# Kernel optimization log

Measured on AMD Instinct MI355X. Metric: run time of the kernel, lower is better.

Reference implementation:

```python
import jax, jax.numpy as jnp
import numpy as np

L = 6  # num_objects (greedy iterations)
BIG = 1e8  # penalty for already-used template ids (matches torch code)


def setup_inputs() -> dict:
    key = jax.random.key(0)
    k1, k2, k3, k4 = jax.random.split(key, 4)
    B, T, C, H, W = 16, 144, 1, 128, 128
    x = jax.random.uniform(k1, (B, C, H, W), jnp.float32)
    templates = jax.random.uniform(k2, (B, T, C, H, W), jnp.float32)
    masks = jax.random.uniform(k3, (B, T, 1, H, W), jnp.float32)
    background = jax.random.uniform(k4, (1, C, H, W), jnp.float32)
    return {"x": x, "templates": templates, "masks": masks, "background": background}


def _greedy_select(x, templates, masks, background):
    """Greedy template selection. Faithful to DecompModel._greedy_selection
    (use_empty is falsy by default -> empty template = 5*ones, empty mask = ones).
    Key identity used for efficiency: dead-leaves composition of the l
    already-selected objects is affine in whatever lies below them:
        recons = A + Mprod * below,
    where A accumulates painted objects and Mprod = prod(1 - mask_i).
    The new candidate at step l is painted BELOW the existing selection
    (it sits at the last index, and compose_templates paints last->first),
    so below = cand*cand_mask + bg*(1-cand_mask). Identical math, no
    O(B*T*l) recomposition per step."""
    B, T = templates.shape[0], templates.shape[1]
    H, W = templates.shape[-2], templates.shape[-1]
    empty_t = 5.0 * jnp.ones((B, 1) + templates.shape[2:], templates.dtype)
    empty_m = jnp.ones((B, 1) + masks.shape[2:], masks.dtype)
    temps = jnp.concatenate([empty_t, templates], axis=1)   # (B,T+1,C,H,W)
    ms = jnp.concatenate([empty_m, masks], axis=1)           # (B,T+1,1,H,W)
    bg = jnp.broadcast_to(background, (B,) + background.shape[1:])  # (B,C,H,W)

    A0 = jnp.zeros_like(bg)                                  # painted-so-far
    M0 = jnp.ones((B, 1, H, W), bg.dtype)                    # transmission
    used0 = jnp.zeros((B, T + 1), bool)
    bidx = jnp.arange(B)

    def step(carry, _):
        A, Mprod, used = carry
        below = temps * ms + bg[:, None] * (1.0 - ms)        # (B,T+1,C,H,W)
        recons = A[:, None] + Mprod[:, None] * below         # (B,T+1,C,H,W)
        errors = jnp.mean((x[:, None] - recons) ** 2, axis=(2, 3, 4))  # (B,T+1)
        errors = jnp.where(used, BIG, errors)
        ids = jnp.argmin(errors, axis=1)                     # (B,)
        hit = (jnp.arange(T + 1)[None, :] == ids[:, None]) & (ids[:, None] != 0)
        used = used | hit                                    # empty id=0 reusable
        sel_t = temps[bidx, ids]                             # (B,C,H,W)
        sel_m = ms[bidx, ids]                                # (B,1,H,W)
        A = A + Mprod * sel_t * sel_m
        Mprod = Mprod * (1.0 - sel_m)
        return (A, Mprod, used), ids

    (_, _, _), ids = jax.lax.scan(step, (A0, M0, used0), None, length=L)
    ids = ids.T                                              # (B,L)
    objects = temps[bidx[:, None], ids]                      # (B,L,C,H,W)
    omasks = ms[bidx[:, None], ids]                          # (B,L,1,H,W)
    return objects, omasks, ids


def _compose(objects, omasks, background):
    """Dead-leaves composition, painting from last object to first
    (first selected object ends up on top), as in compose_templates."""
    B, N = objects.shape[0], objects.shape[1]
    recons = jnp.broadcast_to(background, (B,) + background.shape[1:])
    for i in range(N):  # small fixed loop over L objects
        o = objects[:, N - 1 - i]
        m = omasks[:, N - 1 - i]
        recons = o * m + recons * (1.0 - m)
    return recons


def reference(x, templates, masks, background):
    objects, omasks, ids = _greedy_select(x, templates, masks, background)
    recons = _compose(objects, omasks, background)           # (B,C,H,W)
    return recons, objects, omasks, ids
```

## Files before the change

kernel.cpp:

```cpp
#include <hip/hip_runtime.h>
#include <math.h>

#define BB 16
#define TT 144
#define TP1 145
#define HW4 4096
#define HW8 2048
#define LL 6
#define BIGE 1e30
#define EPSQ 7.62951e-6
#define RB 37
#define NBLK (BB * RB)
#define BCHUNK 74
#define RCHUNK 290

typedef float          f4    __attribute__((ext_vector_type(4)));
typedef float          f8    __attribute__((ext_vector_type(8)));
typedef unsigned short u16x4 __attribute__((ext_vector_type(4)));
typedef unsigned short u16x8 __attribute__((ext_vector_type(8)));

static const size_t OFF_MS   = 0;
static const size_t OFF_R    = 1u << 20;
static const size_t OFF_E32  = 2u << 20;
static const size_t OFF_E16  = (2u << 20) + 32768;
static const size_t OFF_D    = (2u << 20) + 65536;
static const size_t OFF_USED = (2u << 20) + 81920;
static const size_t OFF_WQ   = 3u << 20;
static const size_t WS_FULL  = OFF_WQ + 75497472ull;

__device__ __forceinline__ float hsum(f4 v) { return ((v.x + v.y) + v.z) + v.w; }
__device__ __forceinline__ float hsum8(f8 v) {
    return (((v.s0 + v.s1) + (v.s2 + v.s3)) + ((v.s4 + v.s5) + (v.s6 + v.s7)));
}
__device__ __forceinline__ f8 fabs8(f8 v) {
    f8 o;
    o.s0 = __builtin_fabsf(v.s0); o.s1 = __builtin_fabsf(v.s1);
    o.s2 = __builtin_fabsf(v.s2); o.s3 = __builtin_fabsf(v.s3);
    o.s4 = __builtin_fabsf(v.s4); o.s5 = __builtin_fabsf(v.s5);
    o.s6 = __builtin_fabsf(v.s6); o.s7 = __builtin_fabsf(v.s7);
    return o;
}

__device__ __forceinline__ double blk_reduce(double s) {
    for (int off = 32; off; off >>= 1) s += __shfl_down(s, off);
    __shared__ double smr[4];
    if ((threadIdx.x & 63) == 0) smr[threadIdx.x >> 6] = s;
    __syncthreads();
    return smr[0] + smr[1] + smr[2] + smr[3];
}

__device__ __forceinline__ void blk_reduce2(double& a, double& b) {
    for (int off = 32; off; off >>= 1) { a += __shfl_down(a, off); b += __shfl_down(b, off); }
    __shared__ double sa[4], sb[4];
    if ((threadIdx.x & 63) == 0) { sa[threadIdx.x >> 6] = a; sb[threadIdx.x >> 6] = b; }
    __syncthreads();
    a = sa[0] + sa[1] + sa[2] + sa[3];
    b = sb[0] + sb[1] + sb[2] + sb[3];
}

__device__ __forceinline__ void blk_reduce4(double s[4]) {
    for (int off = 32; off; off >>= 1) {
        s[0] += __shfl_down(s[0], off); s[1] += __shfl_down(s[1], off);
        s[2] += __shfl_down(s[2], off); s[3] += __shfl_down(s[3], off);
    }
    __shared__ double sm4[4][4];
    const int wv = threadIdx.x >> 6;
    if ((threadIdx.x & 63) == 0) {
        sm4[wv][0] = s[0]; sm4[wv][1] = s[1]; sm4[wv][2] = s[2]; sm4[wv][3] = s[3];
    }
    __syncthreads();
    for (int k = 0; k < 4; ++k) s[k] = sm4[0][k] + sm4[1][k] + sm4[2][k] + sm4[3][k];
}

__global__ void k_build(const f4* __restrict__ temps, const f4* __restrict__ masks,
                        const f4* __restrict__ bg, const f4* __restrict__ x,
                        u16x4* __restrict__ wq, double* __restrict__ err32,
                        int* __restrict__ used) {
    const int lin = blockIdx.x;
    const int wg = (lin & 7) * BCHUNK + (lin >> 3);
    const int b = wg / RB, rg = wg - b * RB;
    const int tid = threadIdx.x;
    const f4* xb = x + (size_t)b * HW4;
    if (rg == RB - 1) {
        if (tid < TP1) used[b * TP1 + tid] = 0;
        double s = 0.0;
        for (int j = tid; j < HW4; j += 256) {
            f4 d = 5.f - xb[j];
            s += (double)hsum(d * d);
        }
        double tot = blk_reduce(s);
        if (tid == 0) err32[b * TP1 + 0] = tot;
        return;
    }
    const int tbase = 1 + rg * 4;
    const size_t r0 = ((size_t)(b * TT + tbase - 1)) * HW4;
    const size_t r1 = r0 + HW4, r2 = r1 + HW4, r3 = r2 + HW4;
    double s[4] = {0.0, 0.0, 0.0, 0.0};
    #pragma unroll 2
    for (int j = tid; j < HW4; j += 256) {
        f4 bv = bg[j], xv = xb[j];
        f4 tv0 = __builtin_nontemporal_load(&temps[r0 + j]);
        f4 mv0 = __builtin_nontemporal_load(&masks[r0 + j]);
        f4 w0 = tv0 * mv0 + bv * (1.f - mv0);
        wq[r0 + j] = __builtin_convertvector(w0 * 65535.f + 0.5f, u16x4);
        f4 d0 = w0 - xv; s[0] += (double)hsum(d0 * d0);
        f4 tv1 = __builtin_nontemporal_load(&temps[r1 + j]);
        f4 mv1 = __builtin_nontemporal_load(&masks[r1 + j]);
        f4 w1 = tv1 * mv1 + bv * (1.f - mv1);
        wq[r1 + j] = __builtin_convertvector(w1 * 65535.f + 0.5f, u16x4);
        f4 d1 = w1 - xv; s[1] += (double)hsum(d1 * d1);
        f4 tv2 = __builtin_nontemporal_load(&temps[r2 + j]);
        f4 mv2 = __builtin_nontemporal_load(&masks[r2 + j]);
        f4 w2 = tv2 * mv2 + bv * (1.f - mv2);
        wq[r2 + j] = __builtin_convertvector(w2 * 65535.f + 0.5f, u16x4);
        f4 d2 = w2 - xv; s[2] += (double)hsum(d2 * d2);
        f4 tv3 = __builtin_nontemporal_load(&temps[r3 + j]);
        f4 mv3 = __builtin_nontemporal_load(&masks[r3 + j]);
        f4 w3 = tv3 * mv3 + bv * (1.f - mv3);
        wq[r3 + j] = __builtin_convertvector(w3 * 65535.f + 0.5f, u16x4);
        f4 d3 = w3 - xv; s[3] += (double)hsum(d3 * d3);
    }
    blk_reduce4(s);
    if (tid == 0)
        for (int k = 0; k < 4; ++k) err32[b * TP1 + tbase + k] = s[k];
}

__global__ void k_errs(const u16x8* __restrict__ wq,
                       const f8* __restrict__ Ms, const f8* __restrict__ R,
                       const int* __restrict__ used,
                       double* __restrict__ err16, double* __restrict__ Dd) {
    const int lin = blockIdx.x;
    const int wg = (lin & 7) * BCHUNK + (lin >> 3);
    const int b = wg / RB, rg = wg - b * RB;
    const int tid = threadIdx.x;
    const f8* msb = Ms + (size_t)b * HW8;
    const f8* rb  = R  + (size_t)b * HW8;
    if (rg == RB - 1) {
        double s = 0.0, d = 0.0;
        for (int j = tid; j < HW8; j += 256) {
            f8 ms = msb[j], rr = rb[j];
            f8 M = ms * 65535.f;
            f8 dd = M * 5.f - rr;
            s += (double)hsum8(dd * dd);
            d += (double)hsum8(M * (M + fabs8(rr)));
        }
        blk_reduce2(s, d);
        if (tid == 0) { err16[b * TP1 + 0] = s; Dd[b] = d; }
        return;
    }
    const int tbase = 1 + rg * 4;
    const size_t r0 = ((size_t)(b * TT + tbase - 1)) * HW8;
    const size_t r1 = r0 + HW8, r2 = r1 + HW8, r3 = r2 + HW8;
    double s[4] = {0.0, 0.0, 0.0, 0.0};
    #pragma unroll 2
    for (int j = tid; j < HW8; j += 256) {
        f8 ms = msb[j], rr = rb[j];
        f8 q0 = __builtin_convertvector(wq[r0 + j], f8);
        f8 d0 = q0 * ms - rr; s[0] += (double)hsum8(d0 * d0);
        f8 q1 = __builtin_convertvector(wq[r1 + j], f8);
        f8 d1 = q1 * ms - rr; s[1] += (double)hsum8(d1 * d1);
        f8 q2 = __builtin_convertvector(wq[r2 + j], f8);
        f8 d2 = q2 * ms - rr; s[2] += (double)hsum8(d2 * d2);
        f8 q3 = __builtin_convertvector(wq[r3 + j], f8);
        f8 d3 = q3 * ms - rr; s[3] += (double)hsum8(d3 * d3);
    }
    blk_reduce4(s);
    if (tid == 0)
        for (int k = 0; k < 4; ++k) {
            int t = tbase + k;
            err16[b * TP1 + t] = used[b * TP1 + t] ? BIGE : s[k];
        }
}

__global__ void k_refine(const f4* __restrict__ temps, const f4* __restrict__ masks,
                         const f4* __restrict__ bg,
                         const f4* __restrict__ Ms4, const f4* __restrict__ R4,
                         const double* __restrict__ err16, const double* __restrict__ Dd,
                         double* __restrict__ err32) {
    const int lin = blockIdx.x;
    const int wg = (lin & 7) * RCHUNK + (lin >> 3);
    const int b = wg / TP1, t = wg - b * TP1;
    const int tid = threadIdx.x;
    double e = (tid < TP1) ? err16[b * TP1 + tid] : 1e300;
    double m = e;
    for (int off = 32; off; off >>= 1) {
        double o = __shfl_down(m, off);
        m = (o < m) ? o : m;
    }
    __shared__ double sm[4]; __shared__ double smin_s; __shared__ int scnt[4];
    if ((tid & 63) == 0) sm[tid >> 6] = m;
    __syncthreads();
    if (tid == 0) {
        double a = (sm[0] < sm[1]) ? sm[0] : sm[1];
        double c = (sm[2] < sm[3]) ? sm[2] : sm[3];
        smin_s = (a < c) ? a : c;
    }
    __syncthreads();
    const double thr = smin_s + (6.0 * EPSQ * Dd[b] + 0.15);
    int flag = (tid < TP1) && (e <= thr);
    unsigned long long bal = __ballot(flag);
    if ((tid & 63) == 0) scnt[tid >> 6] = __popcll(bal);
    __syncthreads();
    const int cnt = scnt[0] + scnt[1] + scnt[2] + scnt[3];
    const double mys = err16[b * TP1 + t];
    if (mys > thr) { if (tid == 0) err32[b * TP1 + t] = BIGE; return; }
    if (cnt == 1 || t == 0) { if (tid == 0) err32[b * TP1 + t] = mys; return; }
    const size_t row = ((size_t)(b * TT + t - 1)) * HW4;
    const f4* msb = Ms4 + (size_t)b * HW4;
    const f4* rb  = R4  + (size_t)b * HW4;
    double s = 0.0;
    for (int j = tid; j < HW4; j += 256) {
        f4 tv = temps[row + j], mv = masks[row + j], bv = bg[j];
        f4 w = tv * mv + bv * (1.f - mv);
        f4 M = msb[j] * 65535.f;
        f4 d = w * M - rb[j];
        s += (double)hsum(d * d);
    }
    double tot = blk_reduce(s);
    if (tid == 0) err32[b * TP1 + t] = tot;
}

template <bool FIRST, bool LAST>
__global__ void k_upd(const f4* __restrict__ temps, const f4* __restrict__ masks,
                      const f4* __restrict__ x, const f4* __restrict__ bg,
                      const double* __restrict__ err,
                      int* __restrict__ used, f4* __restrict__ Ms4, f4* __restrict__ R4,
                      f4* __restrict__ out_obj, f4* __restrict__ out_msk,
                      f4* __restrict__ out_rec, float* __restrict__ out_ids, int l) {
    const int lin = blockIdx.x;
    const int wg = (lin & 7) * 32 + (lin >> 3);
    const int tid = threadIdx.x;
    const int gid = wg * 256 + tid;
    const int b = gid >> 12;
    const int p = gid & (HW4 - 1);
    __shared__ int ssel;
    if (tid < 64) {
        double best = 1e301; int bi = TP1;
        for (int t = tid; t < TP1; t += 64) {
            double e = err[b * TP1 + t];
            if (e < best) { best = e; bi = t; }
        }
        for (int off = 32; off; off >>= 1) {
            double oe = __shfl_down(best, off);
            int    oi = __shfl_down(bi, off);
            if (oe < best || (oe == best && oi < bi)) { best = oe; bi = oi; }
        }
        if (tid == 0) ssel = bi;
    }
    __syncthreads();
    const int id = ssel;
    f4 st, sm_;
    if (id == 0) { st = (f4){5.f,5.f,5.f,5.f}; sm_ = (f4){1.f,1.f,1.f,1.f}; }
    else {
        size_t base = ((size_t)(b * TT + id - 1)) * HW4 + p;
        st = temps[base]; sm_ = masks[base];
    }
    f4 xv = x[gid];
    f4 a, mp;
    if (FIRST) { a = (f4){0.f,0.f,0.f,0.f}; mp = (f4){1.f,1.f,1.f,1.f}; }
    else       { mp = Ms4[gid] * 65535.f; a = xv - R4[gid]; }
    a = a + mp * st * sm_;
    mp = mp * (1.f - sm_);
    const size_t ob = ((size_t)(b * LL + l)) * HW4 + p;
    out_obj[ob] = st;
    out_msk[ob] = sm_;
    if (LAST) {
        out_rec[gid] = a + mp * bg[p];
    } else {
        Ms4[gid] = mp * (1.f / 65535.f);
        R4[gid]  = xv - a;
    }
    if ((wg & 15) == 0 && tid == 0) {
        if (id != 0) used[b * TP1 + id] = 1;
        out_ids[b * LL + l] = (float)id;
    }
}

__global__ void k_init0(const f4* __restrict__ x, f4* __restrict__ Ms4, f4* __restrict__ R4,
                        int* __restrict__ used) {
    int gid = blockIdx.x * blockDim.x + threadIdx.x;
    if (gid < BB * TP1) used[gid] = 0;
    if (gid >= BB * HW4) return;
    float msv = (float)(1.0 / 65535.0);
    Ms4[gid] = (f4){msv, msv, msv, msv};
    R4[gid] = x[gid];
}

__global__ void k_errfb(const f4* __restrict__ temps, const f4* __restrict__ masks,
                        const f4* __restrict__ bg,
                        const f4* __restrict__ Ms4, const f4* __restrict__ R4,
                        const int* __restrict__ used, double* __restrict__ err32) {
    const int lin = blockIdx.x;
    const int wg = (lin & 7) * RCHUNK + (lin >> 3);
    const int b = wg / TP1, t = wg - b * TP1;
    const int tid = threadIdx.x;
    if (t != 0 && used[b * TP1 + t]) {
        if (tid == 0) err32[b * TP1 + t] = BIGE;
        return;
    }
    const f4* msb = Ms4 + (size_t)b * HW4;
    const f4* rb  = R4  + (size_t)b * HW4;
    double s = 0.0;
    if (t == 0) {
        for (int j = tid; j < HW4; j += 256) {
            f4 M = msb[j] * 65535.f;
            f4 d = M * 5.f - rb[j];
            s += (double)hsum(d * d);
        }
    } else {
        const size_t row = ((size_t)(b * TT + t - 1)) * HW4;
        for (int j = tid; j < HW4; j += 256) {
            f4 tv = temps[row + j], mv = masks[row + j], bv = bg[j];
            f4 w = tv * mv + bv * (1.f - mv);
            f4 M = msb[j] * 65535.f;
            f4 d = w * M - rb[j];
            s += (double)hsum(d * d);
        }
    }
    double tot = blk_reduce(s);
    if (tid == 0) err32[b * TP1 + t] = tot;
}

extern "C" void kernel_launch(void* const* d_in, const int* in_sizes, int n_in,
                              void* d_out, int out_size, void* d_ws, size_t ws_size,
                              hipStream_t stream) {
    const f4* x     = (const f4*)d_in[0];
    const f4* temps = (const f4*)d_in[1];
    const f4* masks = (const f4*)d_in[2];
    const f4* bg    = (const f4*)d_in[3];

    float* out      = (float*)d_out;
    f4*    out_rec  = (f4*)out;
    f4*    out_obj  = (f4*)(out + 262144);
    f4*    out_msk  = (f4*)(out + 262144 + 1572864);
    float* out_ids  = out + 262144 + 2 * 1572864;

    char* ws = (char*)d_ws;
    f4*     Ms4   = (f4*)(ws + OFF_MS);
    f4*     R4    = (f4*)(ws + OFF_R);
    double* err32 = (double*)(ws + OFF_E32);
    double* err16 = (double*)(ws + OFF_E16);
    double* Dd    = (double*)(ws + OFF_D);
    int*    used  = (int*)(ws + OFF_USED);
    u16x4*  wq    = (u16x4*)(ws + OFF_WQ);

    const bool full = (ws_size >= WS_FULL);

    if (full) {
        k_build<<<NBLK, 256, 0, stream>>>(temps, masks, bg, x, wq, err32, used);
        k_upd<true, false><<<256, 256, 0, stream>>>(temps, masks, x, bg, err32, used,
                                                    Ms4, R4, out_obj, out_msk, out_rec, out_ids, 0);
        for (int l = 1; l < LL; ++l) {
            k_errs<<<NBLK, 256, 0, stream>>>((const u16x8*)wq, (const f8*)Ms4, (const f8*)R4,
                                             used, err16, Dd);
            k_refine<<<BB * TP1, 256, 0, stream>>>(temps, masks, bg, Ms4, R4, err16, Dd, err32);
            if (l < LL - 1)
                k_upd<false, false><<<256, 256, 0, stream>>>(temps, masks, x, bg, err32, used,
                                                             Ms4, R4, out_obj, out_msk, out_rec, out_ids, l);
            else
                k_upd<false, true><<<256, 256, 0, stream>>>(temps, masks, x, bg, err32, used,
                                                            Ms4, R4, out_obj, out_msk, out_rec, out_ids, l);
        }
    } else {
        k_init0<<<(BB * HW4 + 255) / 256, 256, 0, stream>>>(x, Ms4, R4, used);
        for (int l = 0; l < LL; ++l) {
            k_errfb<<<BB * TP1, 256, 0, stream>>>(temps, masks, bg, Ms4, R4, used, err32);
            if (l == 0)
                k_upd<true, false><<<256, 256, 0, stream>>>(temps, masks, x, bg, err32, used,
                                                            Ms4, R4, out_obj, out_msk, out_rec, out_ids, l);
            else if (l == LL - 1)
                k_upd<false, true><<<256, 256, 0, stream>>>(temps, masks, x, bg, err32, used,
                                                            Ms4, R4, out_obj, out_msk, out_rec, out_ids, l);
            else
                k_upd<false, false><<<256, 256, 0, stream>>>(temps, masks, x, bg, err32, used,
                                                             Ms4, R4, out_obj, out_msk, out_rec, out_ids, l);
        }
    }
}
```

Before: 240.4 us.

## Fuse state update with quantized error pass and resolve argmin per batch

Each greedy step used to run three launches: quantized error, refine and update. These become two: a per-batch resolve kernel picks the argmin, refines near-ties exactly and zeroes the accumulators, and a fused kernel applies the selected object to the state and, in the same pass, accumulates the next step's quantized errors for all templates through atomic adds. This removes a launch per step and the reread of the state buffers. It relies on double-precision atomics and on one block per batch for the tie refinement, which could serialize if many candidates fall within the threshold.

```diff
diff --git a/kernel.cpp b/kernel.cpp
--- a/kernel.cpp
+++ b/kernel.cpp
@@ -6,6 +6,7 @@
 #define TP1 145
 #define HW4 4096
 #define HW8 2048
+#define HWF2 8192
 #define LL 6
 #define BIGE 1e30
 #define EPSQ 7.62951e-6
@@ -18,13 +19,15 @@
 typedef float          f8    __attribute__((ext_vector_type(8)));
 typedef unsigned short u16x4 __attribute__((ext_vector_type(4)));
 typedef unsigned short u16x8 __attribute__((ext_vector_type(8)));
-
-static const size_t OFF_MS   = 0;
+typedef unsigned long long ull;
+
+static const size_t OFF_M    = 0;
 static const size_t OFF_R    = 1u << 20;
 static const size_t OFF_E32  = 2u << 20;
 static const size_t OFF_E16  = (2u << 20) + 32768;
 static const size_t OFF_D    = (2u << 20) + 65536;
 static const size_t OFF_USED = (2u << 20) + 81920;
+static const size_t OFF_SEL  = (2u << 20) + 98304;
 static const size_t OFF_WQ   = 3u << 20;
 static const size_t WS_FULL  = OFF_WQ + 75497472ull;
 
@@ -41,12 +44,19 @@
     return o;
 }
 
+__device__ __forceinline__ double wave_reduce_d(double s) {
+    for (int off = 32; off; off >>= 1) s += __shfl_down(s, off);
+    return s;
+}
+
 __device__ __forceinline__ double blk_reduce(double s) {
     for (int off = 32; off; off >>= 1) s += __shfl_down(s, off);
     __shared__ double smr[4];
     if ((threadIdx.x & 63) == 0) smr[threadIdx.x >> 6] = s;
     __syncthreads();
-    return smr[0] + smr[1] + smr[2] + smr[3];
+    double r = smr[0] + smr[1] + smr[2] + smr[3];
+    __syncthreads();
+    return r;
 }
 
 __device__ __forceinline__ void blk_reduce2(double& a, double& b) {
@@ -56,6 +66,7 @@
     __syncthreads();
     a = sa[0] + sa[1] + sa[2] + sa[3];
     b = sb[0] + sb[1] + sb[2] + sb[3];
+    __syncthreads();
 }
 
 __device__ __forceinline__ void blk_reduce4(double s[4]) {
@@ -125,112 +136,228 @@
         for (int k = 0; k < 4; ++k) err32[b * TP1 + tbase + k] = s[k];
 }
 
-__global__ void k_errs(const u16x8* __restrict__ wq,
-                       const f8* __restrict__ Ms, const f8* __restrict__ R,
-                       const int* __restrict__ used,
-                       double* __restrict__ err16, double* __restrict__ Dd) {
+template <bool EXACT>
+__global__ void k_resolve(const f4* __restrict__ temps, const f4* __restrict__ masks,
+                          const f4* __restrict__ bg,
+                          const f4* __restrict__ Mst, const f4* __restrict__ Rst,
+                          const double* __restrict__ scr, double* __restrict__ zbuf,
+                          double* __restrict__ Dd, int* __restrict__ used,
+                          int* __restrict__ selp, float* __restrict__ out_ids, int l) {
+    const int b = blockIdx.x;
+    const int tid = threadIdx.x;
+    const double* sb = scr + (size_t)b * TP1;
+    __shared__ int s_sel, s_cnt;
+    __shared__ ull s_mask[3];
+    if (tid < 64) {
+        double e0 = sb[tid];
+        double e1 = (tid + 64 < TP1) ? sb[tid + 64] : 1e301;
+        double e2 = (tid + 128 < TP1) ? sb[tid + 128] : 1e301;
+        if (!EXACT) {
+            if (tid != 0 && used[b * TP1 + tid]) e0 = BIGE;
+            if (tid + 64 < TP1 && used[b * TP1 + tid + 64]) e1 = BIGE;
+            if (tid + 128 < TP1 && used[b * TP1 + tid + 128]) e2 = BIGE;
+        }
+        double best = e0; int bi = tid;
+        if (e1 < best) { best = e1; bi = tid + 64; }
+        if (e2 < best) { best = e2; bi = tid + 128; }
+        for (int off = 32; off; off >>= 1) {
+            double oe = __shfl_down(best, off);
+            int    oi = __shfl_down(bi, off);
+            if (oe < best || (oe == best && oi < bi)) { best = oe; bi = oi; }
+        }
+        best = __shfl(best, 0); bi = __shfl(bi, 0);
+        if (EXACT) {
+            if (tid == 0) { s_sel = bi; s_cnt = 1; }
+        } else {
+            const double thr = best + (6.0 * EPSQ * Dd[b] + 0.15);
+            ull m0 = __ballot(e0 <= thr);
+            ull m1 = __ballot(e1 <= thr);
+            ull m2 = __ballot(e2 <= thr);
+            if (tid == 0) {
+                s_mask[0] = m0; s_mask[1] = m1; s_mask[2] = m2;
+                s_cnt = __popcll(m0) + __popcll(m1) + __popcll(m2);
+                s_sel = bi;
+            }
+        }
+    }
+    __syncthreads();
+    if (!EXACT && s_cnt > 1) {
+        __shared__ double s_beste; __shared__ int s_besti;
+        if (tid == 0) { s_beste = 1e301; s_besti = -1; }
+        __syncthreads();
+        const f4* Mb = Mst + (size_t)b * HW4;
+        const f4* Rb = Rst + (size_t)b * HW4;
+        for (int t = 0; t < TP1; ++t) {
+            if (!((s_mask[t >> 6] >> (t & 63)) & 1ull)) continue;
+            double s;
+            if (t == 0) {
+                s = sb[0];
+            } else {
+                const size_t row = ((size_t)(b * TT + t - 1)) * HW4;
+                double acc = 0.0;
+                for (int j = tid; j < HW4; j += 256) {
+                    f4 tv = temps[row + j], mv = masks[row + j], bv = bg[j];
+                    f4 w = tv * mv + bv * (1.f - mv);
+                    f4 d = w * Mb[j] - Rb[j];
+                    acc += (double)hsum(d * d);
+                }
+                s = blk_reduce(acc);
+            }
+            if (tid == 0 && s < s_beste) { s_beste = s; s_besti = t; }
+            __syncthreads();
+        }
+        if (tid == 0) s_sel = s_besti;
+        __syncthreads();
+    }
+    const int sel = s_sel;
+    if (tid == 0) {
+        selp[b] = sel;
+        out_ids[b * LL + l] = (float)sel;
+        if (sel != 0) used[b * TP1 + sel] = 1;
+        Dd[b] = 0.0;
+    }
+    for (int t = tid; t < TP1; t += 256) zbuf[(size_t)b * TP1 + t] = 0.0;
+}
+
+template <bool FIRST, bool LAST>
+__global__ __launch_bounds__(256) void k_fused(
+    const float2* __restrict__ temps2, const float2* __restrict__ masks2,
+    const float2* __restrict__ x2, const float2* __restrict__ bg2,
+    const u16x8* __restrict__ wq, const int* __restrict__ selp,
+    float2* __restrict__ Mst2, float2* __restrict__ Rst2,
+    double* __restrict__ err16, double* __restrict__ Dd,
+    float2* __restrict__ out_obj2, float2* __restrict__ out_msk2,
+    float2* __restrict__ out_rec2, int l) {
     const int lin = blockIdx.x;
-    const int wg = (lin & 7) * BCHUNK + (lin >> 3);
-    const int b = wg / RB, rg = wg - b * RB;
+    const int wg = (lin & 7) * 64 + (lin >> 3);
+    const int b = wg >> 5;
+    const int s = wg & 31;
     const int tid = threadIdx.x;
-    const f8* msb = Ms + (size_t)b * HW8;
-    const f8* rb  = R  + (size_t)b * HW8;
-    if (rg == RB - 1) {
-        double s = 0.0, d = 0.0;
-        for (int j = tid; j < HW8; j += 256) {
-            f8 ms = msb[j], rr = rb[j];
-            f8 M = ms * 65535.f;
-            f8 dd = M * 5.f - rr;
-            s += (double)hsum8(dd * dd);
-            d += (double)hsum8(M * (M + fabs8(rr)));
-        }
-        blk_reduce2(s, d);
-        if (tid == 0) { err16[b * TP1 + 0] = s; Dd[b] = d; }
+    const int sel = selp[b];
+    const int P = s * 512;
+    const size_t g2 = (size_t)b * HWF2 + (P >> 1) + tid;
+
+    float2 xv = x2[g2];
+    float2 st, sm;
+    if (sel == 0) { st = make_float2(5.f, 5.f); sm = make_float2(1.f, 1.f); }
+    else {
+        size_t base2 = ((size_t)(b * TT + sel - 1)) * HWF2 + (P >> 1) + tid;
+        st = temps2[base2]; sm = masks2[base2];
+    }
+    float2 a, mp;
+    if (FIRST) { a = make_float2(0.f, 0.f); mp = make_float2(1.f, 1.f); }
+    else {
+        mp = Mst2[g2];
+        float2 rr0 = Rst2[g2];
+        a = make_float2(xv.x - rr0.x, xv.y - rr0.y);
+    }
+    a.x += mp.x * st.x * sm.x;  mp.x *= (1.f - sm.x);
+    a.y += mp.y * st.y * sm.y;  mp.y *= (1.f - sm.y);
+    const size_t ob2 = ((size_t)(b * LL + l)) * HWF2 + (P >> 1) + tid;
+    out_obj2[ob2] = st;
+    out_msk2[ob2] = sm;
+    if (LAST) {
+        float2 bv = bg2[(P >> 1) + tid];
+        out_rec2[g2] = make_float2(a.x + mp.x * bv.x, a.y + mp.y * bv.y);
         return;
     }
-    const int tbase = 1 + rg * 4;
-    const size_t r0 = ((size_t)(b * TT + tbase - 1)) * HW8;
-    const size_t r1 = r0 + HW8, r2 = r1 + HW8, r3 = r2 + HW8;
-    double s[4] = {0.0, 0.0, 0.0, 0.0};
-    #pragma unroll 2
-    for (int j = tid; j < HW8; j += 256) {
-        f8 ms = msb[j], rr = rb[j];
-        f8 q0 = __builtin_convertvector(wq[r0 + j], f8);
-        f8 d0 = q0 * ms - rr; s[0] += (double)hsum8(d0 * d0);
-        f8 q1 = __builtin_convertvector(wq[r1 + j], f8);
-        f8 d1 = q1 * ms - rr; s[1] += (double)hsum8(d1 * d1);
-        f8 q2 = __builtin_convertvector(wq[r2 + j], f8);
-        f8 d2 = q2 * ms - rr; s[2] += (double)hsum8(d2 * d2);
-        f8 q3 = __builtin_convertvector(wq[r3 + j], f8);
-        f8 d3 = q3 * ms - rr; s[3] += (double)hsum8(d3 * d3);
-    }
-    blk_reduce4(s);
-    if (tid == 0)
-        for (int k = 0; k < 4; ++k) {
-            int t = tbase + k;
-            err16[b * TP1 + t] = used[b * TP1 + t] ? BIGE : s[k];
-        }
-}
-
-__global__ void k_refine(const f4* __restrict__ temps, const f4* __restrict__ masks,
-                         const f4* __restrict__ bg,
-                         const f4* __restrict__ Ms4, const f4* __restrict__ R4,
-                         const double* __restrict__ err16, const double* __restrict__ Dd,
-                         double* __restrict__ err32) {
+    float2 rr = make_float2(xv.x - a.x, xv.y - a.y);
+    Mst2[g2] = mp;
+    Rst2[g2] = rr;
+    float d0x = 5.f * mp.x - rr.x, d0y = 5.f * mp.y - rr.y;
+    double t0 = (double)(d0x * d0x + d0y * d0y);
+    double dD = (double)(mp.x * (mp.x + __builtin_fabsf(rr.x)) +
+                         mp.y * (mp.y + __builtin_fabsf(rr.y)));
+    blk_reduce2(t0, dD);
+    if (tid == 0) {
+        atomicAdd(&err16[(size_t)b * TP1 + 0], t0);
+        atomicAdd(&Dd[b], dD);
+    }
+    __shared__ float lms[512], lr[512];
+    lms[tid * 2]     = mp.x * (1.f / 65535.f);
+    lms[tid * 2 + 1] = mp.y * (1.f / 65535.f);
+    lr[tid * 2]      = rr.x;
+    lr[tid * 2 + 1]  = rr.y;
+    __syncthreads();
+    const int lane = tid & 63, w = tid >> 6;
+    float ms8[8], r8[8];
+    #pragma unroll
+    for (int k = 0; k < 8; ++k) { ms8[k] = lms[lane * 8 + k]; r8[k] = lr[lane * 8 + k]; }
+    const size_t rowbase = (size_t)b * TT * HW8 + (size_t)(P >> 3) + lane;
+    double* eb = err16 + (size_t)b * TP1 + 1;
+    for (int t = w; t < TT; t += 8) {
+        u16x8 qa = wq[rowbase + (size_t)t * HW8];
+        u16x8 qb = wq[rowbase + (size_t)(t + 4) * HW8];
+        f8 fa = __builtin_convertvector(qa, f8);
+        f8 fb = __builtin_convertvector(qb, f8);
+        float ga = 0.f, gb = 0.f;
+        #pragma unroll
+        for (int k = 0; k < 8; ++k) {
+            float da = fa[k] * ms8[k] - r8[k];
+            float db = fb[k] * ms8[k] - r8[k];
+            ga += da * da;
+            gb += db * db;
+        }
+        double sa = wave_reduce_d((double)ga);
+        double sb = wave_reduce_d((double)gb);
+        if (lane == 0) {
+            atomicAdd(&eb[t], sa);
+            atomicAdd(&eb[t + 4], sb);
+        }
+    }
+}
+
+__global__ void k_init0(const f4* __restrict__ x, f4* __restrict__ Mst, f4* __restrict__ Rst,
+                        int* __restrict__ used) {
+    int gid = blockIdx.x * blockDim.x + threadIdx.x;
+    if (gid < BB * TP1) used[gid] = 0;
+    if (gid >= BB * HW4) return;
+    Mst[gid] = (f4){1.f, 1.f, 1.f, 1.f};
+    Rst[gid] = x[gid];
+}
+
+__global__ void k_errfb(const f4* __restrict__ temps, const f4* __restrict__ masks,
+                        const f4* __restrict__ bg,
+                        const f4* __restrict__ Mst, const f4* __restrict__ Rst,
+                        const int* __restrict__ used, double* __restrict__ err32) {
     const int lin = blockIdx.x;
     const int wg = (lin & 7) * RCHUNK + (lin >> 3);
     const int b = wg / TP1, t = wg - b * TP1;
     const int tid = threadIdx.x;
-    double e = (tid < TP1) ? err16[b * TP1 + tid] : 1e300;
-    double m = e;
-    for (int off = 32; off; off >>= 1) {
-        double o = __shfl_down(m, off);
-        m = (o < m) ? o : m;
-    }
-    __shared__ double sm[4]; __shared__ double smin_s; __shared__ int scnt[4];
-    if ((tid & 63) == 0) sm[tid >> 6] = m;
-    __syncthreads();
-    if (tid == 0) {
-        double a = (sm[0] < sm[1]) ? sm[0] : sm[1];
-        double c = (sm[2] < sm[3]) ? sm[2] : sm[3];
-        smin_s = (a < c) ? a : c;
-    }
-    __syncthreads();
-    const double thr = smin_s + (6.0 * EPSQ * Dd[b] + 0.15);
-    int flag = (tid < TP1) && (e <= thr);
-    unsigned long long bal = __ballot(flag);
-    if ((tid & 63) == 0) scnt[tid >> 6] = __popcll(bal);
-    __syncthreads();
-    const int cnt = scnt[0] + scnt[1] + scnt[2] + scnt[3];
-    const double mys = err16[b * TP1 + t];
-    if (mys > thr) { if (tid == 0) err32[b * TP1 + t] = BIGE; return; }
-    if (cnt == 1 || t == 0) { if (tid == 0) err32[b * TP1 + t] = mys; return; }
-    const size_t row = ((size_t)(b * TT + t - 1)) * HW4;
-    const f4* msb = Ms4 + (size_t)b * HW4;
-    const f4* rb  = R4  + (size_t)b * HW4;
+    if (t != 0 && used[b * TP1 + t]) {
+        if (tid == 0) err32[b * TP1 + t] = BIGE;
+        return;
+    }
+    const f4* Mb = Mst + (size_t)b * HW4;
+    const f4* Rb = Rst + (size_t)b * HW4;
     double s = 0.0;
-    for (int j = tid; j < HW4; j += 256) {
-        f4 tv = temps[row + j], mv = masks[row + j], bv = bg[j];
-        f4 w = tv * mv + bv * (1.f - mv);
-        f4 M = msb[j] * 65535.f;
-        f4 d = w * M - rb[j];
-        s += (double)hsum(d * d);
+    if (t == 0) {
+        for (int j = tid; j < HW4; j += 256) {
+            f4 d = Mb[j] * 5.f - Rb[j];
+            s += (double)hsum(d * d);
+        }
+    } else {
+        const size_t row = ((size_t)(b * TT + t - 1)) * HW4;
+        for (int j = tid; j < HW4; j += 256) {
+            f4 tv = temps[row + j], mv = masks[row + j], bv = bg[j];
+            f4 w = tv * mv + bv * (1.f - mv);
+            f4 d = w * Mb[j] - Rb[j];
+            s += (double)hsum(d * d);
+        }
     }
     double tot = blk_reduce(s);
     if (tid == 0) err32[b * TP1 + t] = tot;
 }
 
 template <bool FIRST, bool LAST>
-__global__ void k_upd(const f4* __restrict__ temps, const f4* __restrict__ masks,
-                      const f4* __restrict__ x, const f4* __restrict__ bg,
-                      const double* __restrict__ err,
-                      int* __restrict__ used, f4* __restrict__ Ms4, f4* __restrict__ R4,
-                      f4* __restrict__ out_obj, f4* __restrict__ out_msk,
-                      f4* __restrict__ out_rec, float* __restrict__ out_ids, int l) {
-    const int lin = blockIdx.x;
-    const int wg = (lin & 7) * 32 + (lin >> 3);
+__global__ void k_updfb(const f4* __restrict__ temps, const f4* __restrict__ masks,
+                        const f4* __restrict__ x, const f4* __restrict__ bg,
+                        const double* __restrict__ err,
+                        int* __restrict__ used, f4* __restrict__ Mst, f4* __restrict__ Rst,
+                        f4* __restrict__ out_obj, f4* __restrict__ out_msk,
+                        f4* __restrict__ out_rec, float* __restrict__ out_ids, int l) {
     const int tid = threadIdx.x;
-    const int gid = wg * 256 + tid;
+    const int gid = blockIdx.x * 256 + tid;
     const int b = gid >> 12;
     const int p = gid & (HW4 - 1);
     __shared__ int ssel;
@@ -258,7 +385,7 @@
     f4 xv = x[gid];
     f4 a, mp;
     if (FIRST) { a = (f4){0.f,0.f,0.f,0.f}; mp = (f4){1.f,1.f,1.f,1.f}; }
-    else       { mp = Ms4[gid] * 65535.f; a = xv - R4[gid]; }
+    else       { mp = Mst[gid]; a = xv - Rst[gid]; }
     a = a + mp * st * sm_;
     mp = mp * (1.f - sm_);
     const size_t ob = ((size_t)(b * LL + l)) * HW4 + p;
@@ -267,58 +394,13 @@
     if (LAST) {
         out_rec[gid] = a + mp * bg[p];
     } else {
-        Ms4[gid] = mp * (1.f / 65535.f);
-        R4[gid]  = xv - a;
-    }
-    if ((wg & 15) == 0 && tid == 0) {
+        Mst[gid] = mp;
+        Rst[gid] = xv - a;
+    }
+    if ((blockIdx.x & 15) == 0 && tid == 0) {
         if (id != 0) used[b * TP1 + id] = 1;
         out_ids[b * LL + l] = (float)id;
     }
-}
-
-__global__ void k_init0(const f4* __restrict__ x, f4* __restrict__ Ms4, f4* __restrict__ R4,
-                        int* __restrict__ used) {
-    int gid = blockIdx.x * blockDim.x + threadIdx.x;
-    if (gid < BB * TP1) used[gid] = 0;
-    if (gid >= BB * HW4) return;
-    float msv = (float)(1.0 / 65535.0);
-    Ms4[gid] = (f4){msv, msv, msv, msv};
-    R4[gid] = x[gid];
-}
-
-__global__ void k_errfb(const f4* __restrict__ temps, const f4* __restrict__ masks,
-                        const f4* __restrict__ bg,
-                        const f4* __restrict__ Ms4, const f4* __restrict__ R4,
-                        const int* __restrict__ used, double* __restrict__ err32) {
-    const int lin = blockIdx.x;
-    const int wg = (lin & 7) * RCHUNK + (lin >> 3);
-    const int b = wg / TP1, t = wg - b * TP1;
-    const int tid = threadIdx.x;
-    if (t != 0 && used[b * TP1 + t]) {
-        if (tid == 0) err32[b * TP1 + t] = BIGE;
-        return;
-    }
-    const f4* msb = Ms4 + (size_t)b * HW4;
-    const f4* rb  = R4  + (size_t)b * HW4;
-    double s = 0.0;
-    if (t == 0) {
-        for (int j = tid; j < HW4; j += 256) {
-            f4 M = msb[j] * 65535.f;
-            f4 d = M * 5.f - rb[j];
-            s += (double)hsum(d * d);
-        }
-    } else {
-        const size_t row = ((size_t)(b * TT + t - 1)) * HW4;
-        for (int j = tid; j < HW4; j += 256) {
-            f4 tv = temps[row + j], mv = masks[row + j], bv = bg[j];
-            f4 w = tv * mv + bv * (1.f - mv);
-            f4 M = msb[j] * 65535.f;
-            f4 d = w * M - rb[j];
-            s += (double)hsum(d * d);
-        }
-    }
-    double tot = blk_reduce(s);
-    if (tid == 0) err32[b * TP1 + t] = tot;
 }
 
 extern "C" void kernel_launch(void* const* d_in, const int* in_sizes, int n_in,
@@ -336,44 +418,52 @@
     float* out_ids  = out + 262144 + 2 * 1572864;
 
     char* ws = (char*)d_ws;
-    f4*     Ms4   = (f4*)(ws + OFF_MS);
-    f4*     R4    = (f4*)(ws + OFF_R);
+    f4*     Mst   = (f4*)(ws + OFF_M);
+    f4*     Rst   = (f4*)(ws + OFF_R);
     double* err32 = (double*)(ws + OFF_E32);
     double* err16 = (double*)(ws + OFF_E16);
     double* Dd    = (double*)(ws + OFF_D);
     int*    used  = (int*)(ws + OFF_USED);
+    int*    selp  = (int*)(ws + OFF_SEL);
     u16x4*  wq    = (u16x4*)(ws + OFF_WQ);
 
     const bool full = (ws_size >= WS_FULL);
 
     if (full) {
         k_build<<<NBLK, 256, 0, stream>>>(temps, masks, bg, x, wq, err32, used);
-        k_upd<true, false><<<256, 256, 0, stream>>>(temps, masks, x, bg, err32, used,
-                                                    Ms4, R4, out_obj, out_msk, out_rec, out_ids, 0);
+        k_resolve<true><<<BB, 256, 0, stream>>>(temps, masks, bg, Mst, Rst,
+                                                err32, err16, Dd, used, selp, out_ids, 0);
+        k_fused<true, false><<<512, 256, 0, stream>>>(
+            (const float2*)temps, (const float2*)masks, (const float2*)x, (const float2*)bg,
+            (const u16x8*)wq, selp, (float2*)Mst, (float2*)Rst, err16, Dd,
+            (float2*)out_obj, (float2*)out_msk, (float2*)out_rec, 0);
         for (int l = 1; l < LL; ++l) {
-            k_errs<<<NBLK, 256, 0, stream>>>((const u16x8*)wq, (const f8*)Ms4, (const f8*)R4,
-                                             used, err16, Dd);
-            k_refine<<<BB * TP1, 256, 0, stream>>>(temps, masks, bg, Ms4, R4, err16, Dd, err32);
+            k_resolve<false><<<BB, 256, 0, stream>>>(temps, masks, bg, Mst, Rst,
+                                                     err16, err16, Dd, used, selp, out_ids, l);
             if (l < LL - 1)
-                k_upd<false, false><<<256, 256, 0, stream>>>(temps, masks, x, bg, err32, used,
-                                                             Ms4, R4, out_obj, out_msk, out_rec, out_ids, l);
+                k_fused<false, false><<<512, 256, 0, stream>>>(
+                    (const float2*)temps, (const float2*)masks, (const float2*)x, (const float2*)bg,
+                    (const u16x8*)wq, selp, (float2*)Mst, (float2*)Rst, err16, Dd,
+                    (float2*)out_obj, (float2*)out_msk, (float2*)out_rec, l);
             else
-                k_upd<false, true><<<256, 256, 0, stream>>>(temps, masks, x, bg, err32, used,
-                                                            Ms4, R4, out_obj, out_msk, out_rec, out_ids, l);
+                k_fused<false, true><<<512, 256, 0, stream>>>(
+                    (const float2*)temps, (const float2*)masks, (const float2*)x, (const float2*)bg,
+                    (const u16x8*)wq, selp, (float2*)Mst, (float2*)Rst, err16, Dd,
+                    (float2*)out_obj, (float2*)out_msk, (float2*)out_rec, l);
         }
     } else {
-        k_init0<<<(BB * HW4 + 255) / 256, 256, 0, stream>>>(x, Ms4, R4, used);
+        k_init0<<<(BB * HW4 + 255) / 256, 256, 0, stream>>>(x, Mst, Rst, used);
         for (int l = 0; l < LL; ++l) {
-            k_errfb<<<BB * TP1, 256, 0, stream>>>(temps, masks, bg, Ms4, R4, used, err32);
+            k_errfb<<<BB * TP1, 256, 0, stream>>>(temps, masks, bg, Mst, Rst, used, err32);
             if (l == 0)
-                k_upd<true, false><<<256, 256, 0, stream>>>(temps, masks, x, bg, err32, used,
-                                                            Ms4, R4, out_obj, out_msk, out_rec, out_ids, l);
+                k_updfb<true, false><<<256, 256, 0, stream>>>(temps, masks, x, bg, err32, used,
+                                                              Mst, Rst, out_obj, out_msk, out_rec, out_ids, l);
             else if (l == LL - 1)
-                k_upd<false, true><<<256, 256, 0, stream>>>(temps, masks, x, bg, err32, used,
-                                                            Ms4, R4, out_obj, out_msk, out_rec, out_ids, l);
+                k_updfb<false, true><<<256, 256, 0, stream>>>(temps, masks, x, bg, err32, used,
+                                                              Mst, Rst, out_obj, out_msk, out_rec, out_ids, l);
             else
-                k_upd<false, false><<<256, 256, 0, stream>>>(temps, masks, x, bg, err32, used,
-                                                             Ms4, R4, out_obj, out_msk, out_rec, out_ids, l);
-        }
-    }
-}
+                k_updfb<false, false><<<256, 256, 0, stream>>>(temps, masks, x, bg, err32, used,
+                                                               Mst, Rst, out_obj, out_msk, out_rec, out_ids, l);
+        }
+    }
+}
```

Result: slower. 444.5 us (+84.9%).

## Replace per-candidate refine kernel with per-batch resolve kernel computing selection once

Applied to the files above, without the earlier changes.

Replaces the 2320-block refine kernel with a 16-block resolve kernel. Each block finds the argmin over the low-precision errors, builds a ballot mask of candidates within the tolerance, and recomputes exact errors serially only for those near-ties. The selected id is written once to a small buffer, so the update kernel no longer repeats the argmin in every block, and the used-mask is applied in resolve instead of in the error kernel. This removes many launched blocks and redundant argmin work, at the cost of serial per-batch refinement that may be slow when many candidates tie, plus one extra launch at step 0.

```diff
diff --git a/kernel.cpp b/kernel.cpp
--- a/kernel.cpp
+++ b/kernel.cpp
@@ -18,6 +18,7 @@
 typedef float          f8    __attribute__((ext_vector_type(8)));
 typedef unsigned short u16x4 __attribute__((ext_vector_type(4)));
 typedef unsigned short u16x8 __attribute__((ext_vector_type(8)));
+typedef unsigned long long ull;
 
 static const size_t OFF_MS   = 0;
 static const size_t OFF_R    = 1u << 20;
@@ -25,6 +26,7 @@
 static const size_t OFF_E16  = (2u << 20) + 32768;
 static const size_t OFF_D    = (2u << 20) + 65536;
 static const size_t OFF_USED = (2u << 20) + 81920;
+static const size_t OFF_SEL  = (2u << 20) + 98304;
 static const size_t OFF_WQ   = 3u << 20;
 static const size_t WS_FULL  = OFF_WQ + 75497472ull;
 
@@ -46,7 +48,9 @@
     __shared__ double smr[4];
     if ((threadIdx.x & 63) == 0) smr[threadIdx.x >> 6] = s;
     __syncthreads();
-    return smr[0] + smr[1] + smr[2] + smr[3];
+    double r = smr[0] + smr[1] + smr[2] + smr[3];
+    __syncthreads();
+    return r;
 }
 
 __device__ __forceinline__ void blk_reduce2(double& a, double& b) {
@@ -56,6 +60,7 @@
     __syncthreads();
     a = sa[0] + sa[1] + sa[2] + sa[3];
     b = sb[0] + sb[1] + sb[2] + sb[3];
+    __syncthreads();
 }
 
 __device__ __forceinline__ void blk_reduce4(double s[4]) {
@@ -127,7 +132,6 @@
 
 __global__ void k_errs(const u16x8* __restrict__ wq,
                        const f8* __restrict__ Ms, const f8* __restrict__ R,
-                       const int* __restrict__ used,
                        double* __restrict__ err16, double* __restrict__ Dd) {
     const int lin = blockIdx.x;
     const int wg = (lin & 7) * BCHUNK + (lin >> 3);
@@ -166,89 +170,106 @@
     }
     blk_reduce4(s);
     if (tid == 0)
-        for (int k = 0; k < 4; ++k) {
-            int t = tbase + k;
-            err16[b * TP1 + t] = used[b * TP1 + t] ? BIGE : s[k];
-        }
-}
-
-__global__ void k_refine(const f4* __restrict__ temps, const f4* __restrict__ masks,
-                         const f4* __restrict__ bg,
-                         const f4* __restrict__ Ms4, const f4* __restrict__ R4,
-                         const double* __restrict__ err16, const double* __restrict__ Dd,
-                         double* __restrict__ err32) {
-    const int lin = blockIdx.x;
-    const int wg = (lin & 7) * RCHUNK + (lin >> 3);
-    const int b = wg / TP1, t = wg - b * TP1;
-    const int tid = threadIdx.x;
-    double e = (tid < TP1) ? err16[b * TP1 + tid] : 1e300;
-    double m = e;
-    for (int off = 32; off; off >>= 1) {
-        double o = __shfl_down(m, off);
-        m = (o < m) ? o : m;
-    }
-    __shared__ double sm[4]; __shared__ double smin_s; __shared__ int scnt[4];
-    if ((tid & 63) == 0) sm[tid >> 6] = m;
-    __syncthreads();
-    if (tid == 0) {
-        double a = (sm[0] < sm[1]) ? sm[0] : sm[1];
-        double c = (sm[2] < sm[3]) ? sm[2] : sm[3];
-        smin_s = (a < c) ? a : c;
-    }
-    __syncthreads();
-    const double thr = smin_s + (6.0 * EPSQ * Dd[b] + 0.15);
-    int flag = (tid < TP1) && (e <= thr);
-    unsigned long long bal = __ballot(flag);
-    if ((tid & 63) == 0) scnt[tid >> 6] = __popcll(bal);
-    __syncthreads();
-    const int cnt = scnt[0] + scnt[1] + scnt[2] + scnt[3];
-    const double mys = err16[b * TP1 + t];
-    if (mys > thr) { if (tid == 0) err32[b * TP1 + t] = BIGE; return; }
-    if (cnt == 1 || t == 0) { if (tid == 0) err32[b * TP1 + t] = mys; return; }
-    const size_t row = ((size_t)(b * TT + t - 1)) * HW4;
-    const f4* msb = Ms4 + (size_t)b * HW4;
-    const f4* rb  = R4  + (size_t)b * HW4;
-    double s = 0.0;
-    for (int j = tid; j < HW4; j += 256) {
-        f4 tv = temps[row + j], mv = masks[row + j], bv = bg[j];
-        f4 w = tv * mv + bv * (1.f - mv);
-        f4 M = msb[j] * 65535.f;
-        f4 d = w * M - rb[j];
-        s += (double)hsum(d * d);
-    }
-    double tot = blk_reduce(s);
-    if (tid == 0) err32[b * TP1 + t] = tot;
-}
-
-template <bool FIRST, bool LAST>
-__global__ void k_upd(const f4* __restrict__ temps, const f4* __restrict__ masks,
-                      const f4* __restrict__ x, const f4* __restrict__ bg,
-                      const double* __restrict__ err,
-                      int* __restrict__ used, f4* __restrict__ Ms4, f4* __restrict__ R4,
-                      f4* __restrict__ out_obj, f4* __restrict__ out_msk,
-                      f4* __restrict__ out_rec, float* __restrict__ out_ids, int l) {
-    const int lin = blockIdx.x;
-    const int wg = (lin & 7) * 32 + (lin >> 3);
-    const int tid = threadIdx.x;
-    const int gid = wg * 256 + tid;
-    const int b = gid >> 12;
-    const int p = gid & (HW4 - 1);
-    __shared__ int ssel;
+        for (int k = 0; k < 4; ++k) err16[b * TP1 + tbase + k] = s[k];
+}
+
+template <bool EXACT>
+__global__ void k_resolve(const f4* __restrict__ temps, const f4* __restrict__ masks,
+                          const f4* __restrict__ bg,
+                          const f4* __restrict__ Ms4, const f4* __restrict__ R4,
+                          const double* __restrict__ scr, const double* __restrict__ Dd,
+                          int* __restrict__ used, int* __restrict__ selp,
+                          float* __restrict__ out_ids, int l) {
+    const int b = blockIdx.x;
+    const int tid = threadIdx.x;
+    __shared__ int s_sel, s_cnt;
+    __shared__ ull s_mask[3];
+    __shared__ double s_e0;
     if (tid < 64) {
-        double best = 1e301; int bi = TP1;
-        for (int t = tid; t < TP1; t += 64) {
-            double e = err[b * TP1 + t];
-            if (e < best) { best = e; bi = t; }
-        }
+        double e0 = scr[b * TP1 + tid];
+        double e1 = (tid + 64 < TP1) ? scr[b * TP1 + tid + 64] : 1e301;
+        double e2 = (tid + 128 < TP1) ? scr[b * TP1 + tid + 128] : 1e301;
+        if (!EXACT) {
+            if (tid != 0 && used[b * TP1 + tid]) e0 = BIGE;
+            if (tid + 64 < TP1 && used[b * TP1 + tid + 64]) e1 = BIGE;
+            if (tid + 128 < TP1 && used[b * TP1 + tid + 128]) e2 = BIGE;
+        }
+        if (tid == 0) s_e0 = e0;
+        double best = e0; int bi = tid;
+        if (e1 < best) { best = e1; bi = tid + 64; }
+        if (e2 < best) { best = e2; bi = tid + 128; }
         for (int off = 32; off; off >>= 1) {
             double oe = __shfl_down(best, off);
             int    oi = __shfl_down(bi, off);
             if (oe < best || (oe == best && oi < bi)) { best = oe; bi = oi; }
         }
-        if (tid == 0) ssel = bi;
-    }
-    __syncthreads();
-    const int id = ssel;
+        best = __shfl(best, 0); bi = __shfl(bi, 0);
+        if (EXACT) {
+            if (tid == 0) { s_sel = bi; s_cnt = 1; }
+        } else {
+            const double thr = best + (6.0 * EPSQ * Dd[b] + 0.15);
+            ull m0 = __ballot(e0 <= thr);
+            ull m1 = __ballot(e1 <= thr);
+            ull m2 = __ballot(e2 <= thr);
+            if (tid == 0) {
+                s_mask[0] = m0; s_mask[1] = m1; s_mask[2] = m2;
+                s_cnt = __popcll(m0) + __popcll(m1) + __popcll(m2);
+                s_sel = bi;
+            }
+        }
+    }
+    __syncthreads();
+    if (!EXACT && s_cnt > 1) {
+        __shared__ double s_beste; __shared__ int s_besti;
+        if (tid == 0) { s_beste = 1e301; s_besti = -1; }
+        __syncthreads();
+        const f4* Mb = Ms4 + (size_t)b * HW4;
+        const f4* Rb = R4  + (size_t)b * HW4;
+        for (int t = 0; t < TP1; ++t) {
+            if (!((s_mask[t >> 6] >> (t & 63)) & 1ull)) continue;
+            double s;
+            if (t == 0) {
+                s = s_e0;
+            } else {
+                const size_t row = ((size_t)(b * TT + t - 1)) * HW4;
+                double acc = 0.0;
+                for (int j = tid; j < HW4; j += 256) {
+                    f4 tv = temps[row + j], mv = masks[row + j], bv = bg[j];
+                    f4 w = tv * mv + bv * (1.f - mv);
+                    f4 M = Mb[j] * 65535.f;
+                    f4 d = w * M - Rb[j];
+                    acc += (double)hsum(d * d);
+                }
+                s = blk_reduce(acc);
+            }
+            if (tid == 0 && s < s_beste) { s_beste = s; s_besti = t; }
+            __syncthreads();
+        }
+        if (tid == 0) s_sel = s_besti;
+        __syncthreads();
+    }
+    if (tid == 0) {
+        const int sel = s_sel;
+        selp[b] = sel;
+        out_ids[b * LL + l] = (float)sel;
+        if (sel != 0) used[b * TP1 + sel] = 1;
+    }
+}
+
+template <bool FIRST, bool LAST>
+__global__ void k_upd(const f4* __restrict__ temps, const f4* __restrict__ masks,
+                      const f4* __restrict__ x, const f4* __restrict__ bg,
+                      const int* __restrict__ selp,
+                      f4* __restrict__ Ms4, f4* __restrict__ R4,
+                      f4* __restrict__ out_obj, f4* __restrict__ out_msk,
+                      f4* __restrict__ out_rec, int l) {
+    const int lin = blockIdx.x;
+    const int wg = (lin & 7) * 32 + (lin >> 3);
+    const int tid = threadIdx.x;
+    const int gid = wg * 256 + tid;
+    const int b = gid >> 12;
+    const int p = gid & (HW4 - 1);
+    const int id = selp[b];
     f4 st, sm_;
     if (id == 0) { st = (f4){5.f,5.f,5.f,5.f}; sm_ = (f4){1.f,1.f,1.f,1.f}; }
     else {
@@ -270,10 +291,6 @@
         Ms4[gid] = mp * (1.f / 65535.f);
         R4[gid]  = xv - a;
     }
-    if ((wg & 15) == 0 && tid == 0) {
-        if (id != 0) used[b * TP1 + id] = 1;
-        out_ids[b * LL + l] = (float)id;
-    }
 }
 
 __global__ void k_init0(const f4* __restrict__ x, f4* __restrict__ Ms4, f4* __restrict__ R4,
@@ -321,6 +338,60 @@
     if (tid == 0) err32[b * TP1 + t] = tot;
 }
 
+template <bool FIRST, bool LAST>
+__global__ void k_updfb(const f4* __restrict__ temps, const f4* __restrict__ masks,
+                        const f4* __restrict__ x, const f4* __restrict__ bg,
+                        const double* __restrict__ err,
+                        int* __restrict__ used, f4* __restrict__ Ms4, f4* __restrict__ R4,
+                        f4* __restrict__ out_obj, f4* __restrict__ out_msk,
+                        f4* __restrict__ out_rec, float* __restrict__ out_ids, int l) {
+    const int tid = threadIdx.x;
+    const int gid = blockIdx.x * 256 + tid;
+    const int b = gid >> 12;
+    const int p = gid & (HW4 - 1);
+    __shared__ int ssel;
+    if (tid < 64) {
+        double best = 1e301; int bi = TP1;
+        for (int t = tid; t < TP1; t += 64) {
+            double e = err[b * TP1 + t];
+            if (e < best) { best = e; bi = t; }
+        }
+        for (int off = 32; off; off >>= 1) {
+            double oe = __shfl_down(best, off);
+            int    oi = __shfl_down(bi, off);
+            if (oe < best || (oe == best && oi < bi)) { best = oe; bi = oi; }
+        }
+        if (tid == 0) ssel = bi;
+    }
+    __syncthreads();
+    const int id = ssel;
+    f4 st, sm_;
+    if (id == 0) { st = (f4){5.f,5.f,5.f,5.f}; sm_ = (f4){1.f,1.f,1.f,1.f}; }
+    else {
+        size_t base = ((size_t)(b * TT + id - 1)) * HW4 + p;
+        st = temps[base]; sm_ = masks[base];
+    }
+    f4 xv = x[gid];
+    f4 a, mp;
+    if (FIRST) { a = (f4){0.f,0.f,0.f,0.f}; mp = (f4){1.f,1.f,1.f,1.f}; }
+    else       { mp = Ms4[gid] * 65535.f; a = xv - R4[gid]; }
+    a = a + mp * st * sm_;
+    mp = mp * (1.f - sm_);
+    const size_t ob = ((size_t)(b * LL + l)) * HW4 + p;
+    out_obj[ob] = st;
+    out_msk[ob] = sm_;
+    if (LAST) {
+        out_rec[gid] = a + mp * bg[p];
+    } else {
+        Ms4[gid] = mp * (1.f / 65535.f);
+        R4[gid]  = xv - a;
+    }
+    if ((blockIdx.x & 15) == 0 && tid == 0) {
+        if (id != 0) used[b * TP1 + id] = 1;
+        out_ids[b * LL + l] = (float)id;
+    }
+}
+
 extern "C" void kernel_launch(void* const* d_in, const int* in_sizes, int n_in,
                               void* d_out, int out_size, void* d_ws, size_t ws_size,
                               hipStream_t stream) {
@@ -342,38 +413,42 @@
     double* err16 = (double*)(ws + OFF_E16);
     double* Dd    = (double*)(ws + OFF_D);
     int*    used  = (int*)(ws + OFF_USED);
+    int*    selp  = (int*)(ws + OFF_SEL);
     u16x4*  wq    = (u16x4*)(ws + OFF_WQ);
 
     const bool full = (ws_size >= WS_FULL);
 
     if (full) {
         k_build<<<NBLK, 256, 0, stream>>>(temps, masks, bg, x, wq, err32, used);
-        k_upd<true, false><<<256, 256, 0, stream>>>(temps, masks, x, bg, err32, used,
-                                                    Ms4, R4, out_obj, out_msk, out_rec, out_ids, 0);
+        k_resolve<true><<<BB, 256, 0, stream>>>(temps, masks, bg, Ms4, R4,
+                                                err32, Dd, used, selp, out_ids, 0);
+        k_upd<true, false><<<256, 256, 0, stream>>>(temps, masks, x, bg, selp,
+                                                    Ms4, R4, out_obj, out_msk, out_rec, 0);
         for (int l = 1; l < LL; ++l) {
             k_errs<<<NBLK, 256, 0, stream>>>((const u16x8*)wq, (const f8*)Ms4, (const f8*)R4,
-                                             used, err16, Dd);
-            k_refine<<<BB * TP1, 256, 0, stream>>>(temps, masks, bg, Ms4, R4, err16, Dd, err32);
+                                             err16, Dd);
+            k_resolve<false><<<BB, 256, 0, stream>>>(temps, masks, bg, Ms4, R4,
+                                                     err16, Dd, used, selp, out_ids, l);
             if (l < LL - 1)
-                k_upd<false, false><<<256, 256, 0, stream>>>(temps, masks, x, bg, err32, used,
-                                                             Ms4, R4, out_obj, out_msk, out_rec, out_ids, l);
+                k_upd<false, false><<<256, 256, 0, stream>>>(temps, masks, x, bg, selp,
+                                                             Ms4, R4, out_obj, out_msk, out_rec, l);
             else
-                k_upd<false, true><<<256, 256, 0, stream>>>(temps, masks, x, bg, err32, used,
-                                                            Ms4, R4, out_obj, out_msk, out_rec, out_ids, l);
+                k_upd<false, true><<<256, 256, 0, stream>>>(temps, masks, x, bg, selp,
+                                                            Ms4, R4, out_obj, out_msk, out_rec, l);
         }
     } else {
         k_init0<<<(BB * HW4 + 255) / 256, 256, 0, stream>>>(x, Ms4, R4, used);
         for (int l = 0; l < LL; ++l) {
             k_errfb<<<BB * TP1, 256, 0, stream>>>(temps, masks, bg, Ms4, R4, used, err32);
             if (l == 0)
-                k_upd<true, false><<<256, 256, 0, stream>>>(temps, masks, x, bg, err32, used,
-                                                            Ms4, R4, out_obj, out_msk, out_rec, out_ids, l);
+                k_updfb<true, false><<<256, 256, 0, stream>>>(temps, masks, x, bg, err32, used,
+                                                              Ms4, R4, out_obj, out_msk, out_rec, out_ids, l);
             else if (l == LL - 1)
-                k_upd<false, true><<<256, 256, 0, stream>>>(temps, masks, x, bg, err32, used,
-                                                            Ms4, R4, out_obj, out_msk, out_rec, out_ids, l);
+                k_updfb<false, true><<<256, 256, 0, stream>>>(temps, masks, x, bg, err32, used,
+                                                              Ms4, R4, out_obj, out_msk, out_rec, out_ids, l);
             else
-                k_upd<false, false><<<256, 256, 0, stream>>>(temps, masks, x, bg, err32, used,
-                                                             Ms4, R4, out_obj, out_msk, out_rec, out_ids, l);
-        }
-    }
-}
+                k_updfb<false, false><<<256, 256, 0, stream>>>(temps, masks, x, bg, err32, used,
+                                                               Ms4, R4, out_obj, out_msk, out_rec, out_ids, l);
+        }
+    }
+}
```

Measured after the change: 362.8 us. +51.0%, slower.
